# Performance work log

Measured on AMD Instinct MI355X. Metric: run time of the kernel, lower is better.

The kernel has to match this reference:

```python
import jax, jax.numpy as jnp
import numpy as np

SIGMA = (2.0, 5.0, 10.0, 20.0, 40.0, 60.0)  # RBF bandwidths from __init__
MAX_SEG = 16  # static upper bound on number of class segments (== n classes in gt)


def setup_inputs() -> dict:
    key = jax.random.key(0)
    k1, k2, k3 = jax.random.split(key, 3)
    B, C, H, W = 1, 128, 64, 64
    predict = jax.random.normal(k1, (B, C, H, W), dtype=jnp.float32)
    target = jax.random.normal(k2, (B, C, H, W), dtype=jnp.float32)
    # sorted_randint -> contiguous variable-size class segments, as the torch loop assumes
    gt = jnp.sort(jax.random.randint(k3, (B * H * W,), 0, MAX_SEG)).reshape(B, H, W)
    ignore_mask = jnp.ones((B, H, W), dtype=bool)  # all pixels visible
    return {"predict": predict, "target": target, "gt": gt, "ignore_mask": ignore_mask}


def _sqdist(a, b):
    # ||a_i - b_j||^2 ; prob_mat in the original is -0.5 * this
    aa = jnp.sum(a * a, axis=1)
    bb = jnp.sum(b * b, axis=1)
    return aa[:, None] + bb[None, :] - 2.0 * (a @ b.T)


def reference(predict, target, gt, ignore_mask):
    d = predict.shape[1]
    # [B,C,H,W] -> [V,C]; ignore_mask is all True so visible set == all pixels
    pf = predict.transpose(0, 2, 3, 1).reshape(-1, d)
    tf = target.transpose(0, 2, 3, 1).reshape(-1, d)
    cls = gt.reshape(-1)

    # segment id = index of contiguous class run (what the Python boundary loop computes)
    boundary = (cls[1:] != cls[:-1]).astype(jnp.int32)
    seg = jnp.concatenate([jnp.zeros((1,), jnp.int32), jnp.cumsum(boundary)])
    counts = jax.ops.segment_sum(jnp.ones(seg.shape, predict.dtype), seg, num_segments=MAX_SEG)

    # pairwise squared distances within/between predict and target (shared across segments)
    Dpp = _sqdist(pf, pf)
    Dtt = _sqdist(tf, tf)
    Dpt = _sqdist(pf, tf)

    # Per segment with M=N=n: ww is +1/(2n^2) on pp/tt blocks, -1/(2n^2) on cross blocks,
    # and sum over the tp block equals sum over the pt block. So
    # loss_s = (1/(2 n^2)) * sum_bw sum_{i,j in s} (Kpp + Ktt - 2 Kpt)_{ij}
    C = jnp.zeros_like(Dpp)
    for bw in SIGMA:
        inv = -0.5 / bw  # K = exp(prob/bw) = exp(-||x_i-x_j||^2 / (2 bw))
        C = C + jnp.exp(inv * Dpp) + jnp.exp(inv * Dtt) - 2.0 * jnp.exp(inv * Dpt)

    same = seg[:, None] == seg[None, :]
    C = jnp.where(same, C, 0.0)
    seg_tot = jax.ops.segment_sum(jnp.sum(C, axis=1), seg, num_segments=MAX_SEG)

    denom = jnp.maximum(2.0 * counts * counts, 1.0)
    loss_s = jnp.where(counts > 0, seg_tot / denom, 0.0)
    pos = loss_s > 0
    loss_s = jnp.where(pos, jnp.sqrt(jnp.where(pos, loss_s, 1.0)), 0.0)  # sqrt(loss) if >0 else 0

    class_count = jnp.sum(counts > 0).astype(predict.dtype)
    return jnp.sum(loss_s) / class_count
```

## Files before the change

### kernel.cpp

```cpp
#include <hip/hip_runtime.h>
#include <math.h>

#define NCLS 16
#define TS   64
#define NB2  2048
#define PIXB 16
#define SLOT 64

typedef float vfloat4 __attribute__((ext_vector_type(4), aligned(4)));
typedef short bf16x8 __attribute__((ext_vector_type(8)));
typedef float f32x4  __attribute__((ext_vector_type(4)));
typedef unsigned short u16x8 __attribute__((ext_vector_type(8)));

struct Ctl {
    int counts[NCLS];
    int starts[NCLS + 1];
    int tpc[NCLS];
    int pairBase[NCLS + 1];
};

__device__ __forceinline__ unsigned bf16_hi(float x) {
    unsigned u = __float_as_uint(x);
    return (u + 0x7FFFu + ((u >> 16) & 1u)) >> 16;
}
__device__ __forceinline__ float bf16_f(unsigned h) {
    return __uint_as_float(h << 16);
}

__global__ __launch_bounds__(256) void prep_kernel(
    const float* __restrict__ P, const float* __restrict__ T,
    const int* __restrict__ gt, int V, int D,
    Ctl* __restrict__ ctl,
    float* __restrict__ normP, float* __restrict__ normT,
    unsigned short* __restrict__ XhP, unsigned short* __restrict__ XlP,
    unsigned short* __restrict__ XhT, unsigned short* __restrict__ XlT,
    int nbNorm) {
    const int b = blockIdx.x;
    const int t = threadIdx.x;
    if (b < nbNorm) {
        __shared__ float pP[16][PIXB + 1], pT[16][PIXB + 1];
        const int pix = t & (PIXB - 1);
        const int dl  = t >> 4;
        const int v   = b * PIXB + pix;
        float np = 0.f, nt = 0.f;
        if (v < V) {
            #pragma unroll 4
            for (int d = dl; d < D; d += 16) {
                float x = P[(long)d * V + v]; np += x * x;
                float y = T[(long)d * V + v]; nt += y * y;
            }
        }
        pP[dl][pix] = np; pT[dl][pix] = nt;
        __syncthreads();
        if (t < PIXB && b * PIXB + t < V) {
            float sp = 0.f, st = 0.f;
            #pragma unroll
            for (int k = 0; k < 16; ++k) { sp += pP[k][t]; st += pT[k][t]; }
            normP[b * PIXB + t] = sp;
            normT[b * PIXB + t] = st;
        }
    } else if (b == nbNorm) {
        if (t < NCLS) {
            int lo = 0, hi = V;
            while (lo < hi) {
                int mid = (lo + hi) >> 1;
                if (gt[mid] < t) lo = mid + 1; else hi = mid;
            }
            ctl->starts[t] = lo;
        }
        if (t == 0) ctl->starts[NCLS] = V;
        __syncthreads();
        if (t == 0) {
            int pb = 0;
            for (int c = 0; c < NCLS; ++c) {
                int n = ctl->starts[c + 1] - ctl->starts[c];
                ctl->counts[c] = n;
                int tp = (n + TS - 1) / TS;
                ctl->tpc[c] = tp;
                ctl->pairBase[c] = pb;
                pb += tp * (tp + 1) / 2;
            }
            ctl->pairBase[NCLS] = pb;
        }
    } else {
        const int idx = b - nbNorm - 1;
        const bool isT = idx >= 64;
        const float* S = isT ? T : P;
        unsigned short* Xh = isT ? XhT : XhP;
        unsigned short* Xl = isT ? XlT : XlP;
        const int u   = (idx & 63) * 256 + t;
        const int v0  = (u & 1023) * 4;
        const int d0  = (u >> 10) * 8;
        vfloat4 val[8];
        #pragma unroll
        for (int k = 0; k < 8; ++k)
            val[k] = *(const vfloat4*)&S[(long)(d0 + k) * V + v0];
        #pragma unroll
        for (int i = 0; i < 4; ++i) {
            u16x8 h, l;
            #pragma unroll
            for (int k = 0; k < 8; ++k) {
                unsigned hh = bf16_hi(val[k][i]);
                h[k] = (unsigned short)hh;
                l[k] = (unsigned short)bf16_hi(val[k][i] - bf16_f(hh));
            }
            *(u16x8*)&Xh[(long)(v0 + i) * D + d0] = h;
            *(u16x8*)&Xl[(long)(v0 + i) * D + d0] = l;
        }
    }
}

__global__ __launch_bounds__(64) void mmd_kernel(
    const unsigned short* __restrict__ XhP, const unsigned short* __restrict__ XlP,
    const unsigned short* __restrict__ XhT, const unsigned short* __restrict__ XlT,
    int V, int D, const Ctl* __restrict__ ctl,
    const float* __restrict__ normP, const float* __restrict__ normT,
    float* __restrict__ slots)
{
    const int lane = threadIdx.x;
    const int W8 = ctl->pairBase[NCLS] * 8;
    const float invs[6] = {-0.25f, -0.1f, -0.05f, -0.025f, -0.0125f, -1.0f/120.0f};

    for (int wi = blockIdx.x; wi < W8; wi += gridDim.x) {
        const int w     = wi >> 3;
        const int strip = (wi >> 1) & 3;
        const int csh   = wi & 1;
        int c = 0;
        while (ctl->pairBase[c + 1] <= w) ++c;
        const int tp = ctl->tpc[c];
        int rem = w - ctl->pairBase[c];
        int ti = 0;
        while (rem >= tp - ti) { rem -= (tp - ti); ++ti; }
        const int tj    = ti + rem;
        const float f   = (ti == tj) ? 1.0f : 2.0f;
        const int n     = ctl->counts[c];
        const int start = ctl->starts[c];
        const int i0    = ti * TS + strip * 16;
        const int j0    = tj * TS + csh * 32;

        const int  ko = (lane >> 4) * 8;
        const long aB  = (long)(start + min(i0 +      (lane & 15), n - 1)) * D + ko;
        const long b0B = (long)(start + min(j0 +      (lane & 15), n - 1)) * D + ko;
        const long b1B = (long)(start + min(j0 + 16 + (lane & 15), n - 1)) * D + ko;

        f32x4 aPP[2], aPT[2], aTT[2], aTP[2];
        #pragma unroll
        for (int s = 0; s < 2; ++s) {
            aPP[s] = (f32x4){0.f,0.f,0.f,0.f};
            aPT[s] = (f32x4){0.f,0.f,0.f,0.f};
            aTT[s] = (f32x4){0.f,0.f,0.f,0.f};
            aTP[s] = (f32x4){0.f,0.f,0.f,0.f};
        }

        bf16x8 fA[4], fB0[4], fB1[4], gA[4], gB0[4], gB1[4];
        auto loadF = [&](int dc, bf16x8* A, bf16x8* B0, bf16x8* B1) {
            A[0]  = *(const bf16x8*)&XhP[aB  + dc];
            A[1]  = *(const bf16x8*)&XlP[aB  + dc];
            A[2]  = *(const bf16x8*)&XhT[aB  + dc];
            A[3]  = *(const bf16x8*)&XlT[aB  + dc];
            B0[0] = *(const bf16x8*)&XhP[b0B + dc];
            B0[1] = *(const bf16x8*)&XlP[b0B + dc];
            B0[2] = *(const bf16x8*)&XhT[b0B + dc];
            B0[3] = *(const bf16x8*)&XlT[b0B + dc];
            B1[0] = *(const bf16x8*)&XhP[b1B + dc];
            B1[1] = *(const bf16x8*)&XlP[b1B + dc];
            B1[2] = *(const bf16x8*)&XhT[b1B + dc];
            B1[3] = *(const bf16x8*)&XlT[b1B + dc];
        };
        auto mfmaStep = [&](bf16x8* A, bf16x8* B0, bf16x8* B1) {
            #pragma unroll
            for (int s = 0; s < 2; ++s) {
                bf16x8* B = s ? B1 : B0;
                aPP[s] = __builtin_amdgcn_mfma_f32_16x16x32_bf16(A[0], B[0], aPP[s], 0,0,0);
                aPP[s] = __builtin_amdgcn_mfma_f32_16x16x32_bf16(A[0], B[1], aPP[s], 0,0,0);
                aPP[s] = __builtin_amdgcn_mfma_f32_16x16x32_bf16(A[1], B[0], aPP[s], 0,0,0);
                aPT[s] = __builtin_amdgcn_mfma_f32_16x16x32_bf16(A[0], B[2], aPT[s], 0,0,0);
                aPT[s] = __builtin_amdgcn_mfma_f32_16x16x32_bf16(A[0], B[3], aPT[s], 0,0,0);
                aPT[s] = __builtin_amdgcn_mfma_f32_16x16x32_bf16(A[1], B[2], aPT[s], 0,0,0);
                aTT[s] = __builtin_amdgcn_mfma_f32_16x16x32_bf16(A[2], B[2], aTT[s], 0,0,0);
                aTT[s] = __builtin_amdgcn_mfma_f32_16x16x32_bf16(A[2], B[3], aTT[s], 0,0,0);
                aTT[s] = __builtin_amdgcn_mfma_f32_16x16x32_bf16(A[3], B[2], aTT[s], 0,0,0);
                aTP[s] = __builtin_amdgcn_mfma_f32_16x16x32_bf16(A[2], B[0], aTP[s], 0,0,0);
                aTP[s] = __builtin_amdgcn_mfma_f32_16x16x32_bf16(A[2], B[1], aTP[s], 0,0,0);
                aTP[s] = __builtin_amdgcn_mfma_f32_16x16x32_bf16(A[3], B[0], aTP[s], 0,0,0);
            }
        };

        loadF(0, fA, fB0, fB1);
        #pragma unroll 1
        for (int dc = 0; dc < D; dc += 64) {
            loadF(dc + 32, gA, gB0, gB1);
            mfmaStep(fA, fB0, fB1);
            if (dc + 64 < D) loadF(dc + 64, fA, fB0, fB1);
            mfmaStep(gA, gB0, gB1);
        }

        float total = 0.0f;
        float nPi[4], nTi[4];
        #pragma unroll
        for (int r = 0; r < 4; ++r) {
            const int gi = start + min(i0 + (lane >> 4) * 4 + r, n - 1);
            nPi[r] = normP[gi];
            nTi[r] = normT[gi];
        }
        #pragma unroll
        for (int s = 0; s < 2; ++s) {
            const int jj = j0 + 16 * s + (lane & 15);
            if (jj < n) {
                const float nPj = normP[start + jj];
                const float nTj = normT[start + jj];
                #pragma unroll
                for (int r = 0; r < 4; ++r) {
                    const int ii = i0 + (lane >> 4) * 4 + r;
                    if (ii < n) {
                        float Dpp = nPi[r] + nPj - 2.0f * aPP[s][r];
                        float Dtt = nTi[r] + nTj - 2.0f * aTT[s][r];
                        float Dpt = nPi[r] + nTj - 2.0f * aPT[s][r];
                        float Dtp = nTi[r] + nPj - 2.0f * aTP[s][r];
                        float s6 = 0.0f;
                        #pragma unroll
                        for (int q = 0; q < 6; ++q) {
                            s6 += __expf(invs[q] * Dpp) + __expf(invs[q] * Dtt)
                                - __expf(invs[q] * Dpt) - __expf(invs[q] * Dtp);
                        }
                        total += f * s6;
                    }
                }
            }
        }

        #pragma unroll
        for (int off = 32; off > 0; off >>= 1)
            total += __shfl_down(total, off, 64);
        if (lane == 0)
            atomicAdd(&slots[c * SLOT + (blockIdx.x & (SLOT - 1))], total);
    }
}

__global__ void finalize_kernel(const int* __restrict__ counts,
                                const float* __restrict__ slots,
                                float* __restrict__ out) {
    __shared__ float cs[NCLS];
    const int t = threadIdx.x;
    if (t < NCLS) {
        float s = 0.0f;
        for (int k = 0; k < SLOT; ++k) s += slots[t * SLOT + k];
        cs[t] = s;
    }
    __syncthreads();
    if (t == 0) {
        float loss = 0.0f;
        int k = 0;
        for (int c = 0; c < NCLS; ++c) {
            int n = counts[c];
            if (n > 0) {
                ++k;
                float fn    = (float)n;
                float denom = fmaxf(2.0f * fn * fn, 1.0f);
                float l     = cs[c] / denom;
                if (l > 0.0f) loss += sqrtf(l);
            }
        }
        out[0] = (k > 0) ? (loss / (float)k) : 0.0f;
    }
}

extern "C" void kernel_launch(void* const* d_in, const int* in_sizes, int n_in,
                              void* d_out, int out_size, void* d_ws, size_t ws_size,
                              hipStream_t stream) {
    const float* predict = (const float*)d_in[0];
    const float* target  = (const float*)d_in[1];
    const int*   gt      = (const int*)d_in[2];

    const int V = in_sizes[2];
    const int D = in_sizes[0] / V;

    char* ws = (char*)d_ws;
    Ctl* ctl = (Ctl*)ws;
    size_t off = (sizeof(Ctl) + 255) & ~(size_t)255;
    float* normP = (float*)(ws + off);                 off += (size_t)V * 4;
    float* normT = (float*)(ws + off);                 off += (size_t)V * 4;
    off = (off + 255) & ~(size_t)255;
    float* slots = (float*)(ws + off);                 off += (size_t)NCLS * SLOT * 4;
    off = (off + 255) & ~(size_t)255;
    unsigned short* XhP = (unsigned short*)(ws + off); off += (size_t)V * D * 2;
    unsigned short* XlP = (unsigned short*)(ws + off); off += (size_t)V * D * 2;
    unsigned short* XhT = (unsigned short*)(ws + off); off += (size_t)V * D * 2;
    unsigned short* XlT = (unsigned short*)(ws + off);

    int nbNorm = (V + PIXB - 1) / PIXB;
    prep_kernel<<<nbNorm + 1 + 128, 256, 0, stream>>>(
        predict, target, gt, V, D, ctl, normP, normT,
        XhP, XlP, XhT, XlT, nbNorm);

    mmd_kernel<<<NB2, 64, 0, stream>>>(XhP, XlP, XhT, XlT, V, D, ctl,
                                       normP, normT, slots);

    finalize_kernel<<<1, 64, 0, stream>>>(ctl->counts, slots, (float*)d_out);
}
```

Measured before the change: 86.65 us.

## Fuse norm computation with bf16 split transpose via shared-memory staging

The prep kernel used to read the inputs twice: once in narrow per-pixel blocks to compute norms, and once in separate blocks to split into bf16 hi/lo and transpose. Now each block handles 64 pixels of one tensor. It loads float4 rows once, computes the norms and the hi/lo split together, stages the transposed data in shared memory, and writes 16-byte coalesced rows. This removes a full second read of the inputs and improves write coalescing, at the cost of more shared memory per block and a hardcoded limit of D at most 128 for the staging buffer.

```diff
diff --git a/kernel.cpp b/kernel.cpp
--- a/kernel.cpp
+++ b/kernel.cpp
@@ -4,13 +4,12 @@
 #define NCLS 16
 #define TS   64
 #define NB2  2048
-#define PIXB 16
 #define SLOT 64
+#define PXB  64
 
 typedef float vfloat4 __attribute__((ext_vector_type(4), aligned(4)));
 typedef short bf16x8 __attribute__((ext_vector_type(8)));
 typedef float f32x4  __attribute__((ext_vector_type(4)));
-typedef unsigned short u16x8 __attribute__((ext_vector_type(8)));
 
 struct Ctl {
     int counts[NCLS];
@@ -34,32 +33,66 @@
     float* __restrict__ normP, float* __restrict__ normT,
     unsigned short* __restrict__ XhP, unsigned short* __restrict__ XlP,
     unsigned short* __restrict__ XhT, unsigned short* __restrict__ XlT,
-    int nbNorm) {
+    int nbT) {
     const int b = blockIdx.x;
     const int t = threadIdx.x;
-    if (b < nbNorm) {
-        __shared__ float pP[16][PIXB + 1], pT[16][PIXB + 1];
-        const int pix = t & (PIXB - 1);
+    if (b < 2 * nbT) {
+        const bool isT = b >= nbT;
+        const float* S = isT ? T : P;
+        unsigned short* Xh = isT ? XhT : XhP;
+        unsigned short* Xl = isT ? XlT : XlP;
+        float* nrm = isT ? normT : normP;
+        const int pb = (b - (isT ? nbT : 0)) * PXB;
+
+        __shared__ unsigned short sH[PXB][136], sL[PXB][136];
+        __shared__ float pn[16][PXB + 4];
+
+        const int px4 = (t & 15) * 4;
         const int dl  = t >> 4;
-        const int v   = b * PIXB + pix;
-        float np = 0.f, nt = 0.f;
-        if (v < V) {
-            #pragma unroll 4
-            for (int d = dl; d < D; d += 16) {
-                float x = P[(long)d * V + v]; np += x * x;
-                float y = T[(long)d * V + v]; nt += y * y;
-            }
-        }
-        pP[dl][pix] = np; pT[dl][pix] = nt;
+        float np[4] = {0.f, 0.f, 0.f, 0.f};
+        const bool full = (pb + px4 + 3 < V);
+        #pragma unroll 1
+        for (int k = 0; dl + 16 * k < D; ++k) {
+            const int d = dl + 16 * k;
+            vfloat4 x;
+            if (full) {
+                x = *(const vfloat4*)&S[(long)d * V + pb + px4];
+            } else {
+                #pragma unroll
+                for (int i = 0; i < 4; ++i)
+                    x[i] = (pb + px4 + i < V) ? S[(long)d * V + pb + px4 + i] : 0.f;
+            }
+            #pragma unroll
+            for (int i = 0; i < 4; ++i) {
+                unsigned hh = bf16_hi(x[i]);
+                sH[px4 + i][d] = (unsigned short)hh;
+                sL[px4 + i][d] = (unsigned short)bf16_hi(x[i] - bf16_f(hh));
+                np[i] += x[i] * x[i];
+            }
+        }
+        #pragma unroll
+        for (int i = 0; i < 4; ++i) pn[dl][px4 + i] = np[i];
         __syncthreads();
-        if (t < PIXB && b * PIXB + t < V) {
-            float sp = 0.f, st = 0.f;
+        if (t < PXB && pb + t < V) {
+            float s = 0.f;
             #pragma unroll
-            for (int k = 0; k < 16; ++k) { sp += pP[k][t]; st += pT[k][t]; }
-            normP[b * PIXB + t] = sp;
-            normT[b * PIXB + t] = st;
-        }
-    } else if (b == nbNorm) {
+            for (int k = 0; k < 16; ++k) s += pn[k][t];
+            nrm[pb + t] = s;
+        }
+        const int px = t >> 2;
+        const int sg = (t & 3) * 32;
+        if (pb + px < V && sg < D) {
+            unsigned short* dh = &Xh[(long)(pb + px) * D + sg];
+            unsigned short* dl2 = &Xl[(long)(pb + px) * D + sg];
+            #pragma unroll
+            for (int q = 0; q < 4; ++q) {
+                if (sg + 8 * q < D) {
+                    *(uint4*)&dh[8 * q]  = *(const uint4*)&sH[px][sg + 8 * q];
+                    *(uint4*)&dl2[8 * q] = *(const uint4*)&sL[px][sg + 8 * q];
+                }
+            }
+        }
+    } else {
         if (t < NCLS) {
             int lo = 0, hi = V;
             while (lo < hi) {
@@ -71,41 +104,16 @@
         if (t == 0) ctl->starts[NCLS] = V;
         __syncthreads();
         if (t == 0) {
-            int pb = 0;
+            int pb2 = 0;
             for (int c = 0; c < NCLS; ++c) {
                 int n = ctl->starts[c + 1] - ctl->starts[c];
                 ctl->counts[c] = n;
                 int tp = (n + TS - 1) / TS;
                 ctl->tpc[c] = tp;
-                ctl->pairBase[c] = pb;
-                pb += tp * (tp + 1) / 2;
-            }
-            ctl->pairBase[NCLS] = pb;
-        }
-    } else {
-        const int idx = b - nbNorm - 1;
-        const bool isT = idx >= 64;
-        const float* S = isT ? T : P;
-        unsigned short* Xh = isT ? XhT : XhP;
-        unsigned short* Xl = isT ? XlT : XlP;
-        const int u   = (idx & 63) * 256 + t;
-        const int v0  = (u & 1023) * 4;
-        const int d0  = (u >> 10) * 8;
-        vfloat4 val[8];
-        #pragma unroll
-        for (int k = 0; k < 8; ++k)
-            val[k] = *(const vfloat4*)&S[(long)(d0 + k) * V + v0];
-        #pragma unroll
-        for (int i = 0; i < 4; ++i) {
-            u16x8 h, l;
-            #pragma unroll
-            for (int k = 0; k < 8; ++k) {
-                unsigned hh = bf16_hi(val[k][i]);
-                h[k] = (unsigned short)hh;
-                l[k] = (unsigned short)bf16_hi(val[k][i] - bf16_f(hh));
-            }
-            *(u16x8*)&Xh[(long)(v0 + i) * D + d0] = h;
-            *(u16x8*)&Xl[(long)(v0 + i) * D + d0] = l;
+                ctl->pairBase[c] = pb2;
+                pb2 += tp * (tp + 1) / 2;
+            }
+            ctl->pairBase[NCLS] = pb2;
         }
     }
 }
@@ -288,10 +296,10 @@
     unsigned short* XhT = (unsigned short*)(ws + off); off += (size_t)V * D * 2;
     unsigned short* XlT = (unsigned short*)(ws + off);
 
-    int nbNorm = (V + PIXB - 1) / PIXB;
-    prep_kernel<<<nbNorm + 1 + 128, 256, 0, stream>>>(
+    int nbT = (V + PXB - 1) / PXB;
+    prep_kernel<<<2 * nbT + 1, 256, 0, stream>>>(
         predict, target, gt, V, D, ctl, normP, normT,
-        XhP, XlP, XhT, XlT, nbNorm);
+        XhP, XlP, XhT, XlT, nbT);
 
     mmd_kernel<<<NB2, 64, 0, stream>>>(XhP, XlP, XhT, XlT, V, D, ctl,
                                        normP, normT, slots);
```

Result: no change. 86.42 us (-0.3%).
